# Kernel optimization log

Measured on AMD Instinct MI355X. Metric: run time of the kernel, lower is better.

The kernel has to match this reference:

```python
import jax, jax.numpy as jnp
import numpy as np

B, S, D, N, L, V = 2, 512, 1024, 4096, 4, 32000
EPS = 1e-5

def ternarize(w):
    # BitNet b1.58-style: scale = mean |w|, quantize to {-1,0,1}, rescale.
    s = jnp.mean(jnp.abs(w)) + 1e-8
    return s * jnp.round(jnp.clip(w / s, -1.0, 1.0))

def tern_ste(w):
    # straight-through estimator (faithful to ternary training)
    return w + jax.lax.stop_gradient(ternarize(w) - w)

def layer_norm(x, g, b):
    mu = jnp.mean(x, axis=-1, keepdims=True)
    var = jnp.var(x, axis=-1, keepdims=True)
    return (x - mu) * jax.lax.rsqrt(var + EPS) * g + b

def setup_inputs() -> dict:
    key = jax.random.key(0)
    ks = jax.random.split(key, 20)
    sc = lambda d: 1.0 / np.sqrt(d)
    inp = {
        'input_ids': jax.random.randint(ks[0], (B, S), 0, V, dtype=jnp.int32),
        'emb':       jax.random.normal(ks[1], (V, D), jnp.float32) * 0.02,
        'pos_emb':   jax.random.normal(ks[2], (S, D), jnp.float32) * 0.02,
        'gru_wih':   jax.random.normal(ks[3], (3 * D, D), jnp.float32) * sc(D),
        'gru_whh':   jax.random.normal(ks[4], (3 * D, D), jnp.float32) * sc(D),
        'gru_bih':   jnp.zeros((3 * D,), jnp.float32),
        'gru_bhh':   jnp.zeros((3 * D,), jnp.float32),
        'syn_w':     jax.random.normal(ks[5], (L, N, D), jnp.float32) * sc(D),
        'syn_b':     jnp.zeros((L, N), jnp.float32),
        'out_w':     jax.random.normal(ks[6], (L, D, N), jnp.float32) * sc(N),
        'out_b':     jnp.zeros((L, D), jnp.float32),
        'ln_g':      jnp.ones((L, D), jnp.float32),
        'ln_b':      jnp.zeros((L, D), jnp.float32),
        'on_g':      jnp.ones((D,), jnp.float32),
        'on_b':      jnp.zeros((D,), jnp.float32),
        'head_w':    jax.random.normal(ks[7], (V, D), jnp.float32) * sc(D),
        'head_b':    jnp.zeros((V,), jnp.float32),
    }
    return inp

def gru(x, wih, whh, bih, bhh):
    # x: [B,S,D] -> [B,S,D], torch nn.GRU semantics, h0 = 0
    # Precompute input projections for all timesteps: [B,S,3D]
    gi_all = jnp.einsum('bsd,ed->bse', x, wih) + bih
    def step(h, gi):
        gh = h @ whh.T + bhh
        ir, iz, inn = jnp.split(gi, 3, axis=-1)
        hr, hz, hn = jnp.split(gh, 3, axis=-1)
        r = jax.nn.sigmoid(ir + hr)
        z = jax.nn.sigmoid(iz + hz)
        n = jnp.tanh(inn + r * hn)
        h_new = (1.0 - z) * n + z * h
        return h_new, h_new
    h0 = jnp.zeros((x.shape[0], whh.shape[1]), x.dtype)
    _, hs = jax.lax.scan(step, h0, jnp.swapaxes(gi_all, 0, 1))
    return jnp.swapaxes(hs, 0, 1)

def reference(input_ids, emb, pos_emb, gru_wih, gru_whh, gru_bih, gru_bhh,
              syn_w, syn_b, out_w, out_b, ln_g, ln_b, on_g, on_b,
              head_w, head_b):
    # Ternary embedding lookup
    x = tern_ste(emb)[input_ids]                       # [B,S,D]
    x = x + pos_emb[None, :x.shape[1], :]
    x = gru(x, gru_wih, gru_whh, gru_bih, gru_bhh)
    for l in range(L):
        residual = x
        hidden = jax.nn.relu(jnp.einsum('bsd,nd->bsn', x, tern_ste(syn_w[l])) + syn_b[l])
        out = jnp.einsum('bsn,dn->bsd', hidden, tern_ste(out_w[l])) + out_b[l]
        x = layer_norm(residual + out, ln_g[l], ln_b[l])
    x = layer_norm(x, on_g, on_b)
    logits = jnp.einsum('bsd,vd->bsv', x, tern_ste(head_w)) + head_b  # [B,S,V]
    return logits
```

## Files before the change

### kernel.cpp

```cpp
#include <hip/hip_runtime.h>
#include <hip/hip_bf16.h>
#include <cstdint>
#include <cstddef>

#define Dm 1024
#define Sm 512
#define Bm 2
#define Nm 4096
#define Lm 4
#define Vm 32000

typedef __attribute__((ext_vector_type(8))) short short8;
typedef __attribute__((ext_vector_type(4))) float floatx4;

__device__ __forceinline__ unsigned short f2b(float f){
  union { float f; unsigned u; } v; v.f = f;
  unsigned r = (v.u + 0x7fffu + ((v.u >> 16) & 1u)) >> 16;
  return (unsigned short)r;
}
__device__ __forceinline__ float b2f(unsigned short h){
  union { unsigned u; float f; } v; v.u = ((unsigned)h) << 16;
  return v.f;
}

__device__ __forceinline__ void gload16(const unsigned short* g, unsigned short* l){
  __builtin_amdgcn_global_load_lds(
      (const __attribute__((address_space(1))) void*)g,
      (__attribute__((address_space(3))) void*)l, 16, 0, 0);
}

__global__ __launch_bounds__(256) void absum_all_kernel(
    const float* __restrict__ emb, const float* __restrict__ syn_w,
    const float* __restrict__ out_w, const float* __restrict__ head_w,
    double* __restrict__ partial)
{
  int wid = blockIdx.x >> 7;
  int blk = blockIdx.x & 127;
  const float* base; long n4;
  if (wid == 0){ base = emb; n4 = (long)Vm * Dm / 4; }
  else if (wid <= 4){ base = syn_w + (size_t)(wid - 1) * Nm * Dm; n4 = (long)Nm * Dm / 4; }
  else if (wid <= 8){ base = out_w + (size_t)(wid - 5) * Dm * Nm; n4 = (long)Nm * Dm / 4; }
  else { base = head_w; n4 = (long)Vm * Dm / 4; }

  long i = (long)blk * 256 + threadIdx.x;
  const long stride = 128L * 256;
  double s = 0.0;
  for (; i < n4; i += stride){
    float4 v = ((const float4*)base)[i];
    s += (double)fabsf(v.x) + (double)fabsf(v.y) + (double)fabsf(v.z) + (double)fabsf(v.w);
  }
  #pragma unroll
  for (int off = 32; off; off >>= 1) s += __shfl_down(s, off, 64);
  __shared__ double wsum[4];
  int lane = threadIdx.x & 63, wv = threadIdx.x >> 6;
  if (lane == 0) wsum[wv] = s;
  __syncthreads();
  if (threadIdx.x == 0) partial[wid * 128 + blk] = wsum[0] + wsum[1] + wsum[2] + wsum[3];
}

__global__ __launch_bounds__(128) void scale_kernel(const double* __restrict__ partials,
                                                    float* __restrict__ scales){
  int b = blockIdx.x;
  int tid = threadIdx.x;
  __shared__ double red[128];
  red[tid] = partials[b * 128 + tid];
  __syncthreads();
  for (int off = 64; off; off >>= 1){
    if (tid < off) red[tid] += red[tid + off];
    __syncthreads();
  }
  if (tid == 0){
    double cnt = (b == 0 || b == 9) ? (double)Vm * (double)Dm : (double)Nm * (double)Dm;
    scales[b] = (float)(red[0] / cnt);
  }
}

__global__ __launch_bounds__(256) void tern_kernel(const float* __restrict__ w,
                                                   const float* __restrict__ smean,
                                                   unsigned short* __restrict__ out, long n4){
  float s = smean[0] + 1e-8f;
  long i = (long)blockIdx.x * blockDim.x + threadIdx.x;
  long stride = (long)gridDim.x * blockDim.x;
  for (; i < n4; i += stride){
    float4 v = ((const float4*)w)[i];
    ushort4 o;
    o.x = f2b(rintf(fminf(fmaxf(v.x / s, -1.f), 1.f)));
    o.y = f2b(rintf(fminf(fmaxf(v.y / s, -1.f), 1.f)));
    o.z = f2b(rintf(fminf(fmaxf(v.z / s, -1.f), 1.f)));
    o.w = f2b(rintf(fminf(fmaxf(v.w / s, -1.f), 1.f)));
    ((ushort4*)out)[i] = o;
  }
}

__global__ __launch_bounds__(256) void split_kernel(const float* __restrict__ w,
                                                    unsigned short* __restrict__ hi,
                                                    unsigned short* __restrict__ lo, long n4){
  long i = (long)blockIdx.x * blockDim.x + threadIdx.x;
  long stride = (long)gridDim.x * blockDim.x;
  for (; i < n4; i += stride){
    float4 v = ((const float4*)w)[i];
    float f[4] = {v.x, v.y, v.z, v.w};
    ushort4 h4, l4;
    unsigned short* hp = (unsigned short*)&h4;
    unsigned short* lp = (unsigned short*)&l4;
    #pragma unroll
    for (int e = 0; e < 4; e++){
      unsigned short h = f2b(f[e]);
      hp[e] = h;
      lp[e] = f2b(f[e] - b2f(h));
    }
    ((ushort4*)hi)[i] = h4;
    ((ushort4*)lo)[i] = l4;
  }
}

__global__ __launch_bounds__(256) void embed_kernel(
    const int* __restrict__ ids, const float* __restrict__ emb,
    const float* __restrict__ pos, const float* __restrict__ smean,
    unsigned short* __restrict__ xhi, unsigned short* __restrict__ xlo)
{
  int row = blockIdx.x;
  int sp  = row & (Sm - 1);
  int id  = ids[row];
  float s = smean[0] + 1e-8f;
  int d = threadIdx.x * 4;
  float4 wv = *(const float4*)(emb + (size_t)id * Dm + d);
  float4 pv = *(const float4*)(pos + (size_t)sp * Dm + d);
  float y[4];
  y[0] = s * rintf(fminf(fmaxf(wv.x / s, -1.f), 1.f)) + pv.x;
  y[1] = s * rintf(fminf(fmaxf(wv.y / s, -1.f), 1.f)) + pv.y;
  y[2] = s * rintf(fminf(fmaxf(wv.z / s, -1.f), 1.f)) + pv.z;
  y[3] = s * rintf(fminf(fmaxf(wv.w / s, -1.f), 1.f)) + pv.w;
  ushort4 h4, l4;
  unsigned short* hp = (unsigned short*)&h4;
  unsigned short* lp = (unsigned short*)&l4;
  #pragma unroll
  for (int e = 0; e < 4; e++){
    unsigned short h = f2b(y[e]);
    hp[e] = h;
    lp[e] = f2b(y[e] - b2f(h));
  }
  size_t base = (size_t)row * Dm + d;
  *(ushort4*)(xhi + base) = h4;
  *(ushort4*)(xlo + base) = l4;
}

template<bool WSPLIT, bool WF32, int BT>
__global__ __launch_bounds__(256) void gemm_kernel(
    const unsigned short* __restrict__ Ahi, const unsigned short* __restrict__ Alo,
    const void* __restrict__ Wsrc, const unsigned short* __restrict__ Wlo,
    const float* __restrict__ bias, const float* __restrict__ smean,
    int relu, float* __restrict__ outf,
    unsigned short* __restrict__ outhi, unsigned short* __restrict__ outlo,
    int M, int N, int K)
{
  constexpr int WT = BT / 2;
  constexpr int FT = WT / 16;
  constexpr int RPT = 256 / BT;
  constexpr int CPT = 32 / RPT;
  constexpr int NU  = CPT / 8;

  __shared__ unsigned short As[2][BT][40];
  __shared__ unsigned short Bs[WSPLIT ? 2 : 1][BT][40];
  int tid = threadIdx.x;
  int wave = tid >> 6, lane = tid & 63;
  int wm = wave >> 1, wn = wave & 1;
  int bm = blockIdx.y, bn = blockIdx.x;

  bool tern = (smean != nullptr);
  float s = 1.f;
  if (tern) s = smean[0] + 1e-8f;

  int arow = tid / RPT, sub = tid % RPT;
  int col0 = sub * CPT;
  const unsigned short* Agh = Ahi + (size_t)(bm * BT + arow) * K + col0;
  const unsigned short* Agl = Alo + (size_t)(bm * BT + arow) * K + col0;
  const float* Wgf = nullptr;
  const unsigned short* Wgh = nullptr;
  const unsigned short* Wgl = nullptr;
  if (WF32) Wgf = (const float*)Wsrc + (size_t)(bn * BT + arow) * K + col0;
  else {
    Wgh = (const unsigned short*)Wsrc + (size_t)(bn * BT + arow) * K + col0;
    if (WSPLIT) Wgl = Wlo + (size_t)(bn * BT + arow) * K + col0;
  }

  floatx4 acc[FT][FT];
  #pragma unroll
  for (int i = 0; i < FT; i++)
    #pragma unroll
    for (int j = 0; j < FT; j++)
      acc[i][j] = (floatx4){0.f, 0.f, 0.f, 0.f};

  int kpb = K / (int)gridDim.z;
  int k_beg = blockIdx.z * kpb;

  for (int k0 = k_beg; k0 < k_beg + kpb; k0 += 32){
    __syncthreads();
    #pragma unroll
    for (int u = 0; u < NU; u++){
      *(uint4*)&As[0][arow][col0 + u * 8] = *(const uint4*)(Agh + k0 + u * 8);
      *(uint4*)&As[1][arow][col0 + u * 8] = *(const uint4*)(Agl + k0 + u * 8);
    }
    if (WF32){
      unsigned short tmp[CPT];
      #pragma unroll
      for (int q = 0; q < CPT / 4; q++){
        float4 wv = *(const float4*)(Wgf + k0 + q * 4);
        float f[4] = {wv.x, wv.y, wv.z, wv.w};
        #pragma unroll
        for (int e = 0; e < 4; e++){
          float w = f[e];
          if (tern) w = rintf(fminf(fmaxf(w / s, -1.f), 1.f));
          tmp[q * 4 + e] = f2b(w);
        }
      }
      #pragma unroll
      for (int u = 0; u < NU; u++)
        *(uint4*)&Bs[0][arow][col0 + u * 8] = *(uint4*)&tmp[u * 8];
    } else {
      #pragma unroll
      for (int u = 0; u < NU; u++){
        *(uint4*)&Bs[0][arow][col0 + u * 8] = *(const uint4*)(Wgh + k0 + u * 8);
        if (WSPLIT)
          *(uint4*)&Bs[1][arow][col0 + u * 8] = *(const uint4*)(Wgl + k0 + u * 8);
      }
    }
    __syncthreads();

    int kq = lane >> 4, mr = lane & 15;
    short8 afh[FT], afl[FT], bfh[FT];
    #pragma unroll
    for (int i = 0; i < FT; i++){
      afh[i] = *(const short8*)&As[0][wm*WT + i*16 + mr][kq*8];
      afl[i] = *(const short8*)&As[1][wm*WT + i*16 + mr][kq*8];
    }
    #pragma unroll
    for (int j = 0; j < FT; j++) bfh[j] = *(const short8*)&Bs[0][wn*WT + j*16 + mr][kq*8];
    #pragma unroll
    for (int i = 0; i < FT; i++)
      #pragma unroll
      for (int j = 0; j < FT; j++){
        acc[i][j] = __builtin_amdgcn_mfma_f32_16x16x32_bf16(afh[i], bfh[j], acc[i][j], 0, 0, 0);
        acc[i][j] = __builtin_amdgcn_mfma_f32_16x16x32_bf16(afl[i], bfh[j], acc[i][j], 0, 0, 0);
      }
    if (WSPLIT){
      short8 bfl[FT];
      #pragma unroll
      for (int j = 0; j < FT; j++) bfl[j] = *(const short8*)&Bs[1][wn*WT + j*16 + mr][kq*8];
      #pragma unroll
      for (int i = 0; i < FT; i++)
        #pragma unroll
        for (int j = 0; j < FT; j++)
          acc[i][j] = __builtin_amdgcn_mfma_f32_16x16x32_bf16(afh[i], bfl[j], acc[i][j], 0, 0, 0);
    }
  }

  bool split = (gridDim.z > 1);
  bool addb = (blockIdx.z == 0);
  int cr = lane >> 4, cc = lane & 15;
  #pragma unroll
  for (int j = 0; j < FT; j++){
    int col = bn * BT + wn * WT + j * 16 + cc;
    float bv = (bias && addb) ? bias[col] : 0.f;
    #pragma unroll
    for (int i = 0; i < FT; i++){
      #pragma unroll
      for (int r = 0; r < 4; r++){
        int row = bm * BT + wm * WT + i * 16 + cr * 4 + r;
        float v = acc[i][j][r] * s + bv;
        if (relu) v = fmaxf(v, 0.f);
        size_t idx = (size_t)row * N + col;
        if (outf){
          if (split) atomicAdd(outf + idx, v);
          else outf[idx] = v;
        }
        if (outhi){
          unsigned short h = f2b(v);
          outhi[idx] = h;
          outlo[idx] = f2b(v - b2f(h));
        }
      }
    }
  }
}

__global__ __launch_bounds__(256) void gemm_lds_kernel(
    const unsigned short* __restrict__ Ahi, const unsigned short* __restrict__ Alo,
    const unsigned short* __restrict__ Whi,
    const float* __restrict__ bias, const float* __restrict__ smean,
    int relu, float* __restrict__ outf, int M, int N, int K)
{
  __shared__ __align__(16) unsigned short lds[3 * 4096];
  int tid = threadIdx.x;
  int wave = tid >> 6, lane = tid & 63;
  int wm = wave >> 1, wn = wave & 1;
  int bm = blockIdx.y, bn = blockIdx.x;

  float s = 1.f;
  if (smean) s = smean[0] + 1e-8f;

  int r0 = wave * 32 + (lane >> 2);
  int r1 = r0 + 16;
  int s0 = (lane & 3) ^ ((r0 >> 1) & 3);
  int s1 = (lane & 3) ^ ((r1 >> 1) & 3);
  const unsigned short* ga0 = Ahi + (size_t)(bm * 128 + r0) * K + s0 * 8;
  const unsigned short* ga1 = Ahi + (size_t)(bm * 128 + r1) * K + s1 * 8;
  const unsigned short* gl0 = Alo + (size_t)(bm * 128 + r0) * K + s0 * 8;
  const unsigned short* gl1 = Alo + (size_t)(bm * 128 + r1) * K + s1 * 8;
  const unsigned short* gw0 = Whi + (size_t)(bn * 128 + r0) * K + s0 * 8;
  const unsigned short* gw1 = Whi + (size_t)(bn * 128 + r1) * K + s1 * 8;
  unsigned short* la = &lds[wave * 1024];

  floatx4 acc[4][4];
  #pragma unroll
  for (int i = 0; i < 4; i++)
    #pragma unroll
    for (int j = 0; j < 4; j++)
      acc[i][j] = (floatx4){0.f, 0.f, 0.f, 0.f};

  for (int k0 = 0; k0 < K; k0 += 32){
    __syncthreads();
    gload16(ga0 + k0, la);
    gload16(ga1 + k0, la + 512);
    gload16(gl0 + k0, la + 4096);
    gload16(gl1 + k0, la + 4096 + 512);
    gload16(gw0 + k0, la + 8192);
    gload16(gw1 + k0, la + 8192 + 512);
    __syncthreads();

    int kq = lane >> 4, mr = lane & 15;
    short8 afh[4], afl[4], bfh[4];
    #pragma unroll
    for (int i = 0; i < 4; i++){
      int r = wm * 64 + i * 16 + mr;
      int off = r * 32 + ((kq ^ ((r >> 1) & 3)) << 3);
      afh[i] = *(const short8*)&lds[off];
      afl[i] = *(const short8*)&lds[4096 + off];
    }
    #pragma unroll
    for (int j = 0; j < 4; j++){
      int r = wn * 64 + j * 16 + mr;
      int off = r * 32 + ((kq ^ ((r >> 1) & 3)) << 3);
      bfh[j] = *(const short8*)&lds[8192 + off];
    }
    #pragma unroll
    for (int i = 0; i < 4; i++)
      #pragma unroll
      for (int j = 0; j < 4; j++){
        acc[i][j] = __builtin_amdgcn_mfma_f32_16x16x32_bf16(afh[i], bfh[j], acc[i][j], 0, 0, 0);
        acc[i][j] = __builtin_amdgcn_mfma_f32_16x16x32_bf16(afl[i], bfh[j], acc[i][j], 0, 0, 0);
      }
  }

  int cr = lane >> 4, cc = lane & 15;
  #pragma unroll
  for (int j = 0; j < 4; j++){
    int col = bn * 128 + wn * 64 + j * 16 + cc;
    float bv = bias ? bias[col] : 0.f;
    #pragma unroll
    for (int i = 0; i < 4; i++){
      #pragma unroll
      for (int r = 0; r < 4; r++){
        int row = bm * 128 + wm * 64 + i * 16 + cr * 4 + r;
        float v = acc[i][j][r] * s + bv;
        if (relu) v = fmaxf(v, 0.f);
        outf[(size_t)row * N + col] = v;
      }
    }
  }
}

__global__ __launch_bounds__(1024) void gru_kernel(
    const float* __restrict__ gi, const float* __restrict__ whh, const float* __restrict__ bhh,
    unsigned long long* __restrict__ hbuf, float* __restrict__ hs,
    unsigned short* __restrict__ xhi, unsigned short* __restrict__ xlo)
{
  __shared__ float lds_h[2 * 1088];
  __shared__ float lds_gh[96];
  int w = blockIdx.x, tid = threadIdx.x;
  int d0 = w * 16;
  int o = tid >> 4, c = tid & 15;
  bool active = (o < 48);
  int g = o >> 4, dl = o & 15;
  int wrow = g * Dm + d0 + dl;
  float wreg[64];
  if (active){
    const float* src = whh + (size_t)wrow * Dm + c * 64;
    #pragma unroll
    for (int i = 0; i < 64; i++) wreg[i] = src[i];
  }
  float bhval = active ? bhh[wrow] : 0.f;

  int bb = tid >> 4, dd = tid & 15;
  float hprev = 0.f;

  for (int t = 0; t < Sm; t++){
    float ir = 0.f, iz = 0.f, inn = 0.f;
    if (tid < 32){
      const float* girow = gi + ((size_t)bb * Sm + t) * (3 * Dm);
      int d = d0 + dd;
      ir  = girow[d];
      iz  = girow[Dm + d];
      inn = girow[2 * Dm + d];
    }
    {
      const unsigned long long* src = hbuf + (size_t)(t & 1) * 2048 + tid * 2;
      unsigned got = 0;
      int spins = 0;
      while (got != 3u){
        #pragma unroll
        for (int q = 0; q < 2; q++){
          if (!(got & (1u << q))){
            unsigned long long wd = __hip_atomic_load(src + q, __ATOMIC_RELAXED,
                                                      __HIP_MEMORY_SCOPE_AGENT);
            if ((unsigned)(wd >> 32) == (unsigned)t){
              union { unsigned u; float f; } cv; cv.u = (unsigned)wd;
              int wi = tid * 2 + q;
              int b = wi >> 10, d = wi & 1023;
              lds_h[b * 1088 + (d >> 6) * 68 + (d & 63)] = cv.f;
              got |= 1u << q;
            }
          }
        }
        if (got != 3u){
          if (++spins > (1 << 20)) break;
          __builtin_amdgcn_s_sleep(1);
        }
      }
    }
    __syncthreads();
    if (active){
      const float* hp = lds_h + c * 68;
      float a0 = 0.f, a1 = 0.f;
      #pragma unroll
      for (int q = 0; q < 16; q++){
        float4 h0 = *(const float4*)(hp + q * 4);
        float4 h1 = *(const float4*)(hp + 1088 + q * 4);
        a0 += wreg[q*4+0] * h0.x; a1 += wreg[q*4+0] * h1.x;
        a0 += wreg[q*4+1] * h0.y; a1 += wreg[q*4+1] * h1.y;
        a0 += wreg[q*4+2] * h0.z; a1 += wreg[q*4+2] * h1.z;
        a0 += wreg[q*4+3] * h0.w; a1 += wreg[q*4+3] * h1.w;
      }
      #pragma unroll
      for (int off = 8; off; off >>= 1){
        a0 += __shfl_xor(a0, off, 16);
        a1 += __shfl_xor(a1, off, 16);
      }
      if (c == 0){
        lds_gh[o]      = a0 + bhval;
        lds_gh[48 + o] = a1 + bhval;
      }
    }
    __syncthreads();
    if (tid < 32){
      float gr = lds_gh[bb * 48 + dd];
      float gz = lds_gh[bb * 48 + 16 + dd];
      float gn = lds_gh[bb * 48 + 32 + dd];
      float rr = 1.f / (1.f + expf(-(ir + gr)));
      float zz = 1.f / (1.f + expf(-(iz + gz)));
      float nn = tanhf(inn + rr * gn);
      float hnew = (1.f - zz) * nn + zz * hprev;
      hprev = hnew;
      int d = d0 + dd;
      union { float f; unsigned u; } cv; cv.f = hnew;
      unsigned long long wd = ((unsigned long long)(unsigned)(t + 1) << 32) | (unsigned long long)cv.u;
      __hip_atomic_store(hbuf + (size_t)((t + 1) & 1) * 2048 + bb * Dm + d, wd,
                         __ATOMIC_RELAXED, __HIP_MEMORY_SCOPE_AGENT);
      size_t oi = ((size_t)bb * Sm + t) * Dm + d;
      hs[oi] = hnew;
      unsigned short h = f2b(hnew);
      xhi[oi] = h;
      xlo[oi] = f2b(hnew - b2f(h));
    }
  }
}

__global__ __launch_bounds__(256) void ln_kernel(
    const float* __restrict__ resid, const float* __restrict__ addv,
    const float* __restrict__ g, const float* __restrict__ b,
    float* __restrict__ outf, unsigned short* __restrict__ outhi,
    unsigned short* __restrict__ outlo)
{
  int row = blockIdx.x;
  int d = threadIdx.x * 4;
  size_t base = (size_t)row * Dm + d;
  float4 v = *(const float4*)(resid + base);
  if (addv){
    float4 a = *(const float4*)(addv + base);
    v.x += a.x; v.y += a.y; v.z += a.z; v.w += a.w;
  }
  float sum = v.x + v.y + v.z + v.w;
  float sq  = v.x*v.x + v.y*v.y + v.z*v.z + v.w*v.w;
  #pragma unroll
  for (int off = 32; off; off >>= 1){
    sum += __shfl_down(sum, off, 64);
    sq  += __shfl_down(sq,  off, 64);
  }
  __shared__ float red[4][2];
  __shared__ float bc[2];
  int lane = threadIdx.x & 63, wv = threadIdx.x >> 6;
  if (lane == 0){ red[wv][0] = sum; red[wv][1] = sq; }
  __syncthreads();
  if (threadIdx.x == 0){
    float st = red[0][0] + red[1][0] + red[2][0] + red[3][0];
    float qt = red[0][1] + red[1][1] + red[2][1] + red[3][1];
    float mu = st * (1.f / Dm);
    float var = qt * (1.f / Dm) - mu * mu;
    bc[0] = mu; bc[1] = rsqrtf(var + 1e-5f);
  }
  __syncthreads();
  float mu = bc[0], rs = bc[1];
  float4 gv = *(const float4*)(g + d);
  float4 bv = *(const float4*)(b + d);
  float y[4];
  y[0] = (v.x - mu) * rs * gv.x + bv.x;
  y[1] = (v.y - mu) * rs * gv.y + bv.y;
  y[2] = (v.z - mu) * rs * gv.z + bv.z;
  y[3] = (v.w - mu) * rs * gv.w + bv.w;
  if (outf) *(float4*)(outf + base) = *(float4*)y;
  if (outhi){
    ushort4 h4, l4;
    unsigned short* hp = (unsigned short*)&h4;
    unsigned short* lp = (unsigned short*)&l4;
    #pragma unroll
    for (int e = 0; e < 4; e++){
      unsigned short h = f2b(y[e]);
      hp[e] = h;
      lp[e] = f2b(y[e] - b2f(h));
    }
    *(ushort4*)(outhi + base) = h4;
    *(ushort4*)(outlo + base) = l4;
  }
}

extern "C" void kernel_launch(void* const* d_in, const int* in_sizes, int n_in,
                              void* d_out, int out_size, void* d_ws, size_t ws_size,
                              hipStream_t stream)
{
  const int*   ids    = (const int*)  d_in[0];
  const float* emb    = (const float*)d_in[1];
  const float* pos    = (const float*)d_in[2];
  const float* wih    = (const float*)d_in[3];
  const float* whh    = (const float*)d_in[4];
  const float* bih    = (const float*)d_in[5];
  const float* bhh    = (const float*)d_in[6];
  const float* syn_w  = (const float*)d_in[7];
  const float* syn_b  = (const float*)d_in[8];
  const float* out_w  = (const float*)d_in[9];
  const float* out_b  = (const float*)d_in[10];
  const float* ln_g   = (const float*)d_in[11];
  const float* ln_b   = (const float*)d_in[12];
  const float* on_g   = (const float*)d_in[13];
  const float* on_b   = (const float*)d_in[14];
  const float* head_w = (const float*)d_in[15];
  const float* head_b = (const float*)d_in[16];
  float* logits = (float*)d_out;

  const size_t MB = (size_t)1 << 20;
  char* ws = (char*)d_ws;
  float*  scales   = (float*) ws;
  double* partials = (double*)(ws + 32768);
  unsigned long long* hbuf = (unsigned long long*)(ws + 131072);
  float*          hs     = (float*)         (ws + 1  * MB);
  unsigned short* xhi    = (unsigned short*)(ws + 5  * MB);
  unsigned short* xlo    = (unsigned short*)(ws + 7  * MB);
  float*          outbuf = (float*)         (ws + 9  * MB);
  float*          gi     = (float*)         (ws + 13 * MB);
  unsigned short* wih_hi = (unsigned short*)(ws + 25 * MB);
  unsigned short* wih_lo = (unsigned short*)(ws + 31 * MB);
  unsigned short* hhi    = (unsigned short*)(ws + 37 * MB);
  unsigned short* hlo    = (unsigned short*)(ws + 45 * MB);
  unsigned short* wbuf   = (unsigned short*)(ws + 53 * MB);

  bool pre_layer = ws_size >= 62  * MB;
  bool pre_head  = ws_size >= 120 * MB;

  hipMemsetAsync(d_ws, 0, 163840, stream);

  absum_all_kernel<<<1280, 256, 0, stream>>>(emb, syn_w, out_w, head_w, partials);
  scale_kernel<<<10, 128, 0, stream>>>(partials, scales);

  embed_kernel<<<1024, 256, 0, stream>>>(ids, emb, pos, scales, xhi, xlo);

  split_kernel<<<2048, 256, 0, stream>>>(wih, wih_hi, wih_lo, (long)(3 * Dm) * Dm / 4);
  gemm_kernel<true, false, 64><<<dim3(3072/64, 1024/64, 1), 256, 0, stream>>>(
      xhi, xlo, wih_hi, wih_lo, bih, nullptr, 0, gi, nullptr, nullptr, 1024, 3072, 1024);

  gru_kernel<<<64, 1024, 0, stream>>>(gi, whh, bhh, hbuf, hs, xhi, xlo);

  for (int l = 0; l < Lm; l++){
    if (pre_layer){
      tern_kernel<<<2048, 256, 0, stream>>>(syn_w + (size_t)l * Nm * Dm, scales + 1 + l,
                                            wbuf, (long)Nm * Dm / 4);
      gemm_kernel<false, false, 64><<<dim3(4096/64, 1024/64, 1), 256, 0, stream>>>(
          xhi, xlo, wbuf, nullptr, syn_b + (size_t)l * Nm, scales + 1 + l,
          1, nullptr, hhi, hlo, 1024, 4096, 1024);
    } else {
      gemm_kernel<false, true, 64><<<dim3(4096/64, 1024/64, 1), 256, 0, stream>>>(
          xhi, xlo, syn_w + (size_t)l * Nm * Dm, nullptr, syn_b + (size_t)l * Nm, scales + 1 + l,
          1, nullptr, hhi, hlo, 1024, 4096, 1024);
    }
    hipMemsetAsync(outbuf, 0, (size_t)1024 * 1024 * 4, stream);
    if (pre_layer){
      tern_kernel<<<2048, 256, 0, stream>>>(out_w + (size_t)l * Dm * Nm, scales + 5 + l,
                                            wbuf, (long)Dm * Nm / 4);
      gemm_kernel<false, false, 64><<<dim3(1024/64, 1024/64, 2), 256, 0, stream>>>(
          hhi, hlo, wbuf, nullptr, out_b + (size_t)l * Dm, scales + 5 + l,
          0, outbuf, nullptr, nullptr, 1024, 1024, 4096);
    } else {
      gemm_kernel<false, true, 64><<<dim3(1024/64, 1024/64, 2), 256, 0, stream>>>(
          hhi, hlo, out_w + (size_t)l * Dm * Nm, nullptr, out_b + (size_t)l * Dm, scales + 5 + l,
          0, outbuf, nullptr, nullptr, 1024, 1024, 4096);
    }
    ln_kernel<<<1024, 256, 0, stream>>>(hs, outbuf, ln_g + (size_t)l * Dm, ln_b + (size_t)l * Dm,
                                        hs, xhi, xlo);
  }
  ln_kernel<<<1024, 256, 0, stream>>>(hs, nullptr, on_g, on_b, nullptr, xhi, xlo);

  if (pre_head){
    tern_kernel<<<2048, 256, 0, stream>>>(head_w, scales + 9, wbuf, (long)Vm * Dm / 4);
    gemm_lds_kernel<<<dim3(32000/128, 1024/128, 1), 256, 0, stream>>>(
        xhi, xlo, wbuf, head_b, scales + 9, 0, logits, 1024, 32000, 1024);
  } else {
    gemm_kernel<false, true, 128><<<dim3(32000/128, 1024/128, 1), 256, 0, stream>>>(
        xhi, xlo, head_w, nullptr, head_b, scales + 9, 0, logits, nullptr, nullptr, 1024, 32000, 1024);
  }
}
```

Baseline: 2.180 ms.

## Overlap weight ternarization with the GRU recurrence using extra blocks

Adds 192 extra blocks to the GRU kernel launch. These blocks ternarize the head weights, and when the workspace is large enough the per-layer syn and out weights too, while the 64 latency-bound GRU blocks run the recurrence. The later standalone tern_kernel launches are dropped when their buffers are already prepared. The aim is to hide weight-conversion bandwidth behind the serial GRU. The risk is that the extra blocks compete for memory bandwidth and CUs with the GRU blocks, which may depend on co-residency and inter-block synchronization.

```diff
diff --git a/kernel.cpp b/kernel.cpp
--- a/kernel.cpp
+++ b/kernel.cpp
@@ -12,6 +12,14 @@
 
 typedef __attribute__((ext_vector_type(8))) short short8;
 typedef __attribute__((ext_vector_type(4))) float floatx4;
+
+struct PrepArgs {
+  const float* src[9];
+  unsigned short* dst[9];
+  long n4[9];
+  int sidx[9];
+  int njobs;
+};
 
 __device__ __forceinline__ unsigned short f2b(float f){
   union { float f; unsigned u; } v; v.f = f;
@@ -370,11 +378,34 @@
   }
 }
 
+#define NGRU 64
 __global__ __launch_bounds__(1024) void gru_kernel(
     const float* __restrict__ gi, const float* __restrict__ whh, const float* __restrict__ bhh,
     unsigned long long* __restrict__ hbuf, float* __restrict__ hs,
-    unsigned short* __restrict__ xhi, unsigned short* __restrict__ xlo)
+    unsigned short* __restrict__ xhi, unsigned short* __restrict__ xlo,
+    const float* __restrict__ scales, PrepArgs pa)
 {
+  if (blockIdx.x >= NGRU){
+    long pid = blockIdx.x - NGRU;
+    long stride = (long)(gridDim.x - NGRU) * 1024;
+    for (int j = 0; j < pa.njobs; j++){
+      float s = scales[pa.sidx[j]] + 1e-8f;
+      const float4* s4 = (const float4*)pa.src[j];
+      ushort4* d4 = (ushort4*)pa.dst[j];
+      long n4 = pa.n4[j];
+      for (long k = pid * 1024 + threadIdx.x; k < n4; k += stride){
+        float4 v = s4[k];
+        ushort4 o;
+        o.x = f2b(rintf(fminf(fmaxf(v.x / s, -1.f), 1.f)));
+        o.y = f2b(rintf(fminf(fmaxf(v.y / s, -1.f), 1.f)));
+        o.z = f2b(rintf(fminf(fmaxf(v.z / s, -1.f), 1.f)));
+        o.w = f2b(rintf(fminf(fmaxf(v.w / s, -1.f), 1.f)));
+        d4[k] = o;
+      }
+    }
+    return;
+  }
+
   __shared__ float lds_h[2 * 1088];
   __shared__ float lds_gh[96];
   int w = blockIdx.x, tid = threadIdx.x;
@@ -566,6 +597,7 @@
   unsigned short* xlo    = (unsigned short*)(ws + 7  * MB);
   float*          outbuf = (float*)         (ws + 9  * MB);
   float*          gi     = (float*)         (ws + 13 * MB);
+  unsigned short* ltbuf  = (unsigned short*)(ws + 13 * MB);
   unsigned short* wih_hi = (unsigned short*)(ws + 25 * MB);
   unsigned short* wih_lo = (unsigned short*)(ws + 31 * MB);
   unsigned short* hhi    = (unsigned short*)(ws + 37 * MB);
@@ -574,6 +606,29 @@
 
   bool pre_layer = ws_size >= 62  * MB;
   bool pre_head  = ws_size >= 120 * MB;
+  bool tier1     = ws_size >= 192 * MB;
+
+  PrepArgs pa; pa.njobs = 0;
+  unsigned short* synp[Lm] = {nullptr, nullptr, nullptr, nullptr};
+  unsigned short* outp[Lm] = {nullptr, nullptr, nullptr, nullptr};
+  auto addjob = [&](const float* s, unsigned short* d, long n4, int si){
+    pa.src[pa.njobs] = s; pa.dst[pa.njobs] = d; pa.n4[pa.njobs] = n4; pa.sidx[pa.njobs] = si;
+    pa.njobs++;
+  };
+  if (pre_head){
+    addjob(head_w, wbuf, (long)Vm * Dm / 4, 9);
+    if (tier1){
+      for (int l = 0; l < Lm; l++){
+        synp[l] = (unsigned short*)(ws + 120 * MB + (size_t)l * 8 * MB);
+        outp[l] = (unsigned short*)(ws + 152 * MB + (size_t)l * 8 * MB);
+        addjob(syn_w + (size_t)l * Nm * Dm, synp[l], (long)Nm * Dm / 4, 1 + l);
+        addjob(out_w + (size_t)l * Dm * Nm, outp[l], (long)Nm * Dm / 4, 5 + l);
+      }
+    } else {
+      synp[0] = (unsigned short*)(ws + 25 * MB);
+      addjob(syn_w, synp[0], (long)Nm * Dm / 4, 1);
+    }
+  }
 
   hipMemsetAsync(d_ws, 0, 163840, stream);
 
@@ -586,28 +641,46 @@
   gemm_kernel<true, false, 64><<<dim3(3072/64, 1024/64, 1), 256, 0, stream>>>(
       xhi, xlo, wih_hi, wih_lo, bih, nullptr, 0, gi, nullptr, nullptr, 1024, 3072, 1024);
 
-  gru_kernel<<<64, 1024, 0, stream>>>(gi, whh, bhh, hbuf, hs, xhi, xlo);
+  gru_kernel<<<NGRU + 192, 1024, 0, stream>>>(gi, whh, bhh, hbuf, hs, xhi, xlo, scales, pa);
 
   for (int l = 0; l < Lm; l++){
-    if (pre_layer){
+    if (pre_head){
+      unsigned short* sw = synp[l];
+      if (!sw){
+        tern_kernel<<<2048, 256, 0, stream>>>(syn_w + (size_t)l * Nm * Dm, scales + 1 + l,
+                                              ltbuf, (long)Nm * Dm / 4);
+        sw = ltbuf;
+      }
+      gemm_kernel<false, false, 64><<<dim3(4096/64, 1024/64, 1), 256, 0, stream>>>(
+          xhi, xlo, sw, nullptr, syn_b + (size_t)l * Nm, scales + 1 + l,
+          1, nullptr, hhi, hlo, 1024, 4096, 1024);
+      hipMemsetAsync(outbuf, 0, (size_t)1024 * 1024 * 4, stream);
+      unsigned short* ow = outp[l];
+      if (!ow){
+        tern_kernel<<<2048, 256, 0, stream>>>(out_w + (size_t)l * Dm * Nm, scales + 5 + l,
+                                              ltbuf, (long)Dm * Nm / 4);
+        ow = ltbuf;
+      }
+      gemm_kernel<false, false, 64><<<dim3(1024/64, 1024/64, 2), 256, 0, stream>>>(
+          hhi, hlo, ow, nullptr, out_b + (size_t)l * Dm, scales + 5 + l,
+          0, outbuf, nullptr, nullptr, 1024, 1024, 4096);
+    } else if (pre_layer){
       tern_kernel<<<2048, 256, 0, stream>>>(syn_w + (size_t)l * Nm * Dm, scales + 1 + l,
                                             wbuf, (long)Nm * Dm / 4);
       gemm_kernel<false, false, 64><<<dim3(4096/64, 1024/64, 1), 256, 0, stream>>>(
           xhi, xlo, wbuf, nullptr, syn_b + (size_t)l * Nm, scales + 1 + l,
           1, nullptr, hhi, hlo, 1024, 4096, 1024);
-    } else {
-      gemm_kernel<false, true, 64><<<dim3(4096/64, 1024/64, 1), 256, 0, stream>>>(
-          xhi, xlo, syn_w + (size_t)l * Nm * Dm, nullptr, syn_b + (size_t)l * Nm, scales + 1 + l,
-          1, nullptr, hhi, hlo, 1024, 4096, 1024);
-    }
-    hipMemsetAsync(outbuf, 0, (size_t)1024 * 1024 * 4, stream);
-    if (pre_layer){
+      hipMemsetAsync(outbuf, 0, (size_t)1024 * 1024 * 4, stream);
       tern_kernel<<<2048, 256, 0, stream>>>(out_w + (size_t)l * Dm * Nm, scales + 5 + l,
                                             wbuf, (long)Dm * Nm / 4);
       gemm_kernel<false, false, 64><<<dim3(1024/64, 1024/64, 2), 256, 0, stream>>>(
           hhi, hlo, wbuf, nullptr, out_b + (size_t)l * Dm, scales + 5 + l,
           0, outbuf, nullptr, nullptr, 1024, 1024, 4096);
     } else {
+      gemm_kernel<false, true, 64><<<dim3(4096/64, 1024/64, 1), 256, 0, stream>>>(
+          xhi, xlo, syn_w + (size_t)l * Nm * Dm, nullptr, syn_b + (size_t)l * Nm, scales + 1 + l,
+          1, nullptr, hhi, hlo, 1024, 4096, 1024);
+      hipMemsetAsync(outbuf, 0, (size_t)1024 * 1024 * 4, stream);
       gemm_kernel<false, true, 64><<<dim3(1024/64, 1024/64, 2), 256, 0, stream>>>(
           hhi, hlo, out_w + (size_t)l * Dm * Nm, nullptr, out_b + (size_t)l * Dm, scales + 5 + l,
           0, outbuf, nullptr, nullptr, 1024, 1024, 4096);
@@ -618,7 +691,6 @@
   ln_kernel<<<1024, 256, 0, stream>>>(hs, nullptr, on_g, on_b, nullptr, xhi, xlo);
 
   if (pre_head){
-    tern_kernel<<<2048, 256, 0, stream>>>(head_w, scales + 9, wbuf, (long)Vm * Dm / 4);
     gemm_lds_kernel<<<dim3(32000/128, 1024/128, 1), 256, 0, stream>>>(
         xhi, xlo, wbuf, head_b, scales + 9, 0, logits, 1024, 32000, 1024);
   } else {
```

After: 2.134 ms. -2.1%, faster.
